# Kernel optimization log

Measured on AMD Instinct MI355X. Metric: run time of the kernel, lower is better.

The kernel has to match this reference:

```python
import jax, jax.numpy as jnp
import numpy as np

# --- constants matching init_kwargs / input_specs ---
B, T, N, C = 16, 60, 196, 512
SEGS, TOP_K, TOP_M = 10, 6, 12
HEADS = 4
HD = C // HEADS  # 128
CLIP = T // SEGS  # 6
FRAMES = CLIP * TOP_K  # 36
LN_EPS = 1e-5


def setup_inputs() -> dict:
    key = jax.random.key(0)
    ks = jax.random.split(key, 16)
    s = 0.02
    return {
        "audio_feat": jax.random.normal(ks[0], (B, T, C), jnp.float32),
        "patch_feat": jax.random.normal(ks[1], (B, T, N, C), jnp.float32),
        "qst_feat": jax.random.normal(ks[2], (B, C), jnp.float32),
        "top_k_index_sort": jnp.sort(jax.random.randint(ks[3], (B, 1, TOP_K), 0, SEGS), axis=-1),
        # MultiheadAttention params (torch layout: in_proj [3C, C])
        "in_proj_w": jax.random.normal(ks[4], (3 * C, C), jnp.float32) * s,
        "in_proj_b": jnp.zeros((3 * C,), jnp.float32),
        "out_w": jax.random.normal(ks[5], (C, C), jnp.float32) * s,
        "out_b": jnp.zeros((C,), jnp.float32),
        # FFN
        "lin1_w": jax.random.normal(ks[6], (C, C), jnp.float32) * s,
        "lin1_b": jnp.zeros((C,), jnp.float32),
        "lin2_w": jax.random.normal(ks[7], (C, C), jnp.float32) * s,
        "lin2_b": jnp.zeros((C,), jnp.float32),
        # LayerNorm
        "ln_g": jnp.ones((C,), jnp.float32),
        "ln_b": jnp.zeros((C,), jnp.float32),
    }


def _layernorm(x, g, b):
    mu = jnp.mean(x, axis=-1, keepdims=True)
    var = jnp.mean(jnp.square(x - mu), axis=-1, keepdims=True)
    return (x - mu) * jax.lax.rsqrt(var + LN_EPS) * g + b


def _forward(audio_feat, patch_feat, qst_feat, top_k_index_sort,
             in_proj_w, in_proj_b, out_w, out_b,
             lin1_w, lin1_b, lin2_w, lin2_b, ln_g, ln_b):
    # --- TopKSegs: gather top-k temporal segments (clip_len frames each) ---
    seg_idx = top_k_index_sort[:, 0, :]  # [B, K]
    frame_ids = (seg_idx[:, :, None] * CLIP + jnp.arange(CLIP)[None, None, :]).reshape(B, FRAMES)
    audio_top_k = jnp.take_along_axis(audio_feat, frame_ids[:, :, None], axis=1)            # [B, F, C]
    patch_top_k = jnp.take_along_axis(patch_feat, frame_ids[:, :, None, None], axis=1)      # [B, F, N, C]

    # --- QstQueryPatchAttn: batched cross-attention (q_len=1 per frame) ---
    Wq, Wk, Wv = in_proj_w[:C], in_proj_w[C:2 * C], in_proj_w[2 * C:]
    bq, bk, bv = in_proj_b[:C], in_proj_b[C:2 * C], in_proj_b[2 * C:]
    q = (qst_feat @ Wq.T + bq).reshape(B, HEADS, HD)                    # [B, h, d]
    k = (patch_top_k @ Wk.T + bk).reshape(B, FRAMES, N, HEADS, HD)      # [B, F, N, h, d]
    v = (patch_top_k @ Wv.T + bv).reshape(B, FRAMES, N, HEADS, HD)
    scale = 1.0 / jnp.sqrt(jnp.asarray(HD, jnp.float32))
    scores = jnp.einsum('bhd,bfnhd->bfhn', q, k) * scale                # [B, F, h, N]
    w = jax.nn.softmax(scores, axis=-1)
    ctx = jnp.einsum('bfhn,bfnhd->bfhd', w, v).reshape(B, FRAMES, C)
    attn_feat = ctx @ out_w.T + out_b                                   # [B, F, C]
    patch_weights = jnp.mean(w, axis=2)                                 # [B, F, N] (avg heads)

    src = jax.nn.relu(attn_feat @ lin1_w.T + lin1_b) @ lin2_w.T + lin2_b
    visual_spatial_feat = _layernorm(attn_feat + src, ln_g, ln_b)       # computed but unused downstream

    # --- SelectTopM (faithful to original loop semantics):
    # top-m indices are sorted ascending and iterated with full-slab overwrite,
    sort_index = jnp.argsort(patch_weights, axis=-1)
    top_m_index = sort_index[:, :, -TOP_M:]
    top_m_index_sort = jnp.sort(top_m_index, axis=-1)
    pid = top_m_index_sort[0, 0, -1]  # last iterated patch id
    sel = jnp.take(patch_top_k, pid, axis=2)                            # [B, F, C]
    visual_patch_top_m = jnp.broadcast_to(sel[:, :, None, :], (B, FRAMES, TOP_M, C))
    visual_patch_feat = visual_patch_top_m.reshape(B, FRAMES * TOP_M, C)
    return audio_top_k, visual_patch_top_m, visual_patch_feat


def reference(audio_feat, patch_feat, qst_feat, top_k_index_sort,
              in_proj_w, in_proj_b, out_w, out_b,
              lin1_w, lin1_b, lin2_w, lin2_b, ln_g, ln_b):
    return _forward(audio_feat, patch_feat, qst_feat, top_k_index_sort,
                    in_proj_w, in_proj_b, out_w, out_b,
                    lin1_w, lin1_b, lin2_w, lin2_b, ln_g, ln_b)
```

## Files before the change

kernel.cpp:

```cpp
#include <hip/hip_runtime.h>
#include <math.h>

#define B_     16
#define T_     60
#define N_     196
#define C_     512
#define SEGS_  10
#define TOPK_  6
#define TOPM_  12
#define HEADS_ 4
#define HD_    128
#define CLIP_  6
#define FRAMES_ 36

#define WS_Q   0
#define WS_SC  512
#define WS_PID 1296

#define SCALE_ 0.08838834764831845f

__global__ void qproj_kernel(const float* __restrict__ qst,
                             const float* __restrict__ ipw,
                             const float* __restrict__ ipb,
                             float* __restrict__ ws) {
    __shared__ float x[C_];
    int tid = threadIdx.x;
    x[tid]       = qst[tid];
    x[tid + 256] = qst[tid + 256];
    __syncthreads();
    const float4* x4 = (const float4*)x;
    for (int r = tid; r < C_; r += 256) {
        const float4* w4 = (const float4*)(ipw + (size_t)r * C_);
        float acc = 0.f;
        #pragma unroll 8
        for (int c = 0; c < C_ / 4; ++c) {
            float4 wv = w4[c], xv = x4[c];
            acc += wv.x * xv.x + wv.y * xv.y + wv.z * xv.z + wv.w * xv.w;
        }
        ws[WS_Q + r] = acc + ipb[r];
    }
}

#define NPER 4
__global__ void score_kernel(const float* __restrict__ patch,
                             const int* __restrict__ tk,
                             const float* __restrict__ ipw,
                             const float* __restrict__ ipb,
                             float* __restrict__ ws) {
    __shared__ float xs[NPER][C_];
    __shared__ float qs[C_];
    __shared__ float kb[NPER][C_];
    int tid = threadIdx.x;
    int n0 = blockIdx.x * NPER;
    int fid0 = tk[0] * CLIP_;
    const size_t base = (size_t)fid0 * N_ * C_;

    qs[tid]       = ws[WS_Q + tid];
    qs[tid + 256] = ws[WS_Q + tid + 256];
    for (int i = tid; i < NPER * C_; i += 256) {
        int n = i >> 9, c = i & (C_ - 1);
        xs[n][c] = patch[base + (size_t)(n0 + n) * C_ + c];
    }
    __syncthreads();

    float a0 = 0.f, a1 = 0.f, a2 = 0.f, a3 = 0.f;
    float b0 = 0.f, b1 = 0.f, b2 = 0.f, b3 = 0.f;
    {
        const float4* w0 = (const float4*)(ipw + (size_t)(C_ + tid) * C_);
        const float4* w1 = (const float4*)(ipw + (size_t)(C_ + tid + 256) * C_);
        const float4* x0 = (const float4*)xs[0];
        const float4* x1 = (const float4*)xs[1];
        const float4* x2 = (const float4*)xs[2];
        const float4* x3 = (const float4*)xs[3];
        for (int c = 0; c < C_ / 4; ++c) {
            float4 wa = w0[c], wb = w1[c];
            float4 v0 = x0[c], v1 = x1[c], v2 = x2[c], v3 = x3[c];
            a0 += wa.x * v0.x + wa.y * v0.y + wa.z * v0.z + wa.w * v0.w;
            a1 += wa.x * v1.x + wa.y * v1.y + wa.z * v1.z + wa.w * v1.w;
            a2 += wa.x * v2.x + wa.y * v2.y + wa.z * v2.z + wa.w * v2.w;
            a3 += wa.x * v3.x + wa.y * v3.y + wa.z * v3.z + wa.w * v3.w;
            b0 += wb.x * v0.x + wb.y * v0.y + wb.z * v0.z + wb.w * v0.w;
            b1 += wb.x * v1.x + wb.y * v1.y + wb.z * v1.z + wb.w * v1.w;
            b2 += wb.x * v2.x + wb.y * v2.y + wb.z * v2.z + wb.w * v2.w;
            b3 += wb.x * v3.x + wb.y * v3.y + wb.z * v3.z + wb.w * v3.w;
        }
    }
    float bk0 = ipb[C_ + tid];
    float bk1 = ipb[C_ + tid + 256];
    kb[0][tid] = a0 + bk0; kb[1][tid] = a1 + bk0;
    kb[2][tid] = a2 + bk0; kb[3][tid] = a3 + bk0;
    kb[0][tid + 256] = b0 + bk1; kb[1][tid + 256] = b1 + bk1;
    kb[2][tid + 256] = b2 + bk1; kb[3][tid + 256] = b3 + bk1;
    __syncthreads();

    int h = tid >> 6, j = tid & 63;
    for (int nn = 0; nn < NPER; ++nn) {
        float p = qs[h * HD_ + j]      * kb[nn][h * HD_ + j]
                + qs[h * HD_ + 64 + j] * kb[nn][h * HD_ + 64 + j];
        for (int off = 32; off; off >>= 1) p += __shfl_down(p, off);
        if (j == 0) ws[WS_SC + h * N_ + n0 + nn] = p * SCALE_;
    }
}

__global__ void pid_kernel(float* __restrict__ ws) {
    __shared__ float wgt[HEADS_][N_];
    __shared__ float pw[N_];
    int tid = threadIdx.x;
    int h = tid >> 6, j = tid & 63;

    float sc[4]; float ex[4];
    int m = 0;
    float mx = -1e30f;
    for (int n = j; n < N_; n += 64) {
        sc[m] = ws[WS_SC + h * N_ + n];
        mx = fmaxf(mx, sc[m]);
        ++m;
    }
    for (int off = 1; off < 64; off <<= 1) mx = fmaxf(mx, __shfl_xor(mx, off));
    float sum = 0.f;
    for (int s = 0; s < m; ++s) { ex[s] = expf(sc[s] - mx); sum += ex[s]; }
    for (int off = 1; off < 64; off <<= 1) sum += __shfl_xor(sum, off);
    float inv = 1.f / sum;
    m = 0;
    for (int n = j; n < N_; n += 64) { wgt[h][n] = ex[m] * inv; ++m; }
    __syncthreads();

    for (int n = tid; n < N_; n += 256)
        pw[n] = 0.25f * (wgt[0][n] + wgt[1][n] + wgt[2][n] + wgt[3][n]);
    __syncthreads();

    if (tid < 64) {
        float v[4];
        for (int s = 0; s < 4; ++s) {
            int n = j + 64 * s;
            v[s] = (n < N_) ? pw[n] : -1e30f;
        }
        int pid = -1;
        for (int r = 0; r < TOPM_; ++r) {
            float bv = -1e30f; int bi = -1;
            for (int s = 0; s < 4; ++s) {
                int n = j + 64 * s;
                if (v[s] > bv || (v[s] == bv && n > bi)) { bv = v[s]; bi = n; }
            }
            for (int off = 1; off < 64; off <<= 1) {
                float ov = __shfl_xor(bv, off);
                int   oi = __shfl_xor(bi, off);
                if (ov > bv || (ov == bv && oi > bi)) { bv = ov; bi = oi; }
            }
            if ((bi & 63) == j) v[bi >> 6] = -1e30f;
            if (bi > pid) pid = bi;
        }
        if (j == 0) ((int*)ws)[WS_PID] = pid;
    }
}

__global__ void out_kernel(const float* __restrict__ audio,
                           const float* __restrict__ patch,
                           const int* __restrict__ tk,
                           const float* __restrict__ ws,
                           float* __restrict__ out) {
    int bf = blockIdx.x;
    int b = bf / FRAMES_, f = bf % FRAMES_;
    int k = f / CLIP_, c = f % CLIP_;
    int fid = tk[b * TOPK_ + k] * CLIP_ + c;
    int t = threadIdx.x;
    int pid = ((const int*)ws)[WS_PID];

    const float4* a4 = (const float4*)(audio + ((size_t)b * T_ + fid) * C_);
    const float4* p4 = (const float4*)(patch + (((size_t)b * T_ + fid) * N_ + pid) * C_);
    float4 av = a4[t];
    float4 sv = p4[t];

    float4* o0 = (float4*)out;
    float4* o1 = (float4*)(out + (size_t)B_ * FRAMES_ * C_);
    float4* o2 = (float4*)(out + (size_t)B_ * FRAMES_ * C_ + (size_t)B_ * FRAMES_ * TOPM_ * C_);

    o0[(size_t)bf * (C_ / 4) + t] = av;
    size_t rb = (size_t)bf * TOPM_ * (C_ / 4);
    #pragma unroll
    for (int mm = 0; mm < TOPM_; ++mm) {
        o1[rb + mm * (C_ / 4) + t] = sv;
        o2[rb + mm * (C_ / 4) + t] = sv;
    }
}

extern "C" void kernel_launch(void* const* d_in, const int* in_sizes, int n_in,
                              void* d_out, int out_size, void* d_ws, size_t ws_size,
                              hipStream_t stream) {
    const float* audio = (const float*)d_in[0];
    const float* patch = (const float*)d_in[1];
    const float* qst   = (const float*)d_in[2];
    const int*   tk    = (const int*)d_in[3];
    const float* ipw   = (const float*)d_in[4];
    const float* ipb   = (const float*)d_in[5];
    float* out = (float*)d_out;
    float* ws  = (float*)d_ws;

    qproj_kernel<<<1, 256, 0, stream>>>(qst, ipw, ipb, ws);
    score_kernel<<<N_ / NPER, 256, 0, stream>>>(patch, tk, ipw, ipb, ws);
    pid_kernel<<<1, 256, 0, stream>>>(ws);
    out_kernel<<<B_ * FRAMES_, 128, 0, stream>>>(audio, patch, tk, ws, out);
}
```

Measured before the change: 529.5 us.

## Fold key projection into query: score patches via q^T Wk instead of full K

```diff
diff --git a/kernel.cpp b/kernel.cpp
--- a/kernel.cpp
+++ b/kernel.cpp
@@ -13,9 +13,9 @@
 #define CLIP_  6
 #define FRAMES_ 36
 
-#define WS_Q   0
-#define WS_SC  512
-#define WS_PID 1296
+#define WS_Q    0
+#define WS_SCP  512
+#define WS_PID  2080
 
 #define SCALE_ 0.08838834764831845f
 
@@ -28,77 +28,56 @@
     x[tid]       = qst[tid];
     x[tid + 256] = qst[tid + 256];
     __syncthreads();
+
+    int wave = tid >> 6, lane = tid & 63;
+    int half = lane >> 5, l = lane & 31;
+    int row = blockIdx.x * 8 + wave * 2 + half;
+
+    const float4* w4 = (const float4*)(ipw + (size_t)row * C_);
     const float4* x4 = (const float4*)x;
-    for (int r = tid; r < C_; r += 256) {
-        const float4* w4 = (const float4*)(ipw + (size_t)r * C_);
-        float acc = 0.f;
-        #pragma unroll 8
-        for (int c = 0; c < C_ / 4; ++c) {
-            float4 wv = w4[c], xv = x4[c];
-            acc += wv.x * xv.x + wv.y * xv.y + wv.z * xv.z + wv.w * xv.w;
-        }
-        ws[WS_Q + r] = acc + ipb[r];
+    float acc = 0.f;
+    #pragma unroll
+    for (int j = 0; j < 4; ++j) {
+        float4 wv = w4[l + 32 * j];
+        float4 xv = x4[l + 32 * j];
+        acc += wv.x * xv.x + wv.y * xv.y + wv.z * xv.z + wv.w * xv.w;
     }
+    for (int off = 16; off; off >>= 1) acc += __shfl_xor(acc, off);
+    if (l == 0) ws[WS_Q + row] = acc + ipb[row];
 }
 
-#define NPER 4
 __global__ void score_kernel(const float* __restrict__ patch,
                              const int* __restrict__ tk,
                              const float* __restrict__ ipw,
-                             const float* __restrict__ ipb,
                              float* __restrict__ ws) {
-    __shared__ float xs[NPER][C_];
-    __shared__ float qs[C_];
-    __shared__ float kb[NPER][C_];
+    __shared__ float qh[HD_];
+    __shared__ float us[256];
     int tid = threadIdx.x;
-    int n0 = blockIdx.x * NPER;
-    int fid0 = tk[0] * CLIP_;
-    const size_t base = (size_t)fid0 * N_ * C_;
+    int h = blockIdx.x >> 1, half = blockIdx.x & 1;
+    int c = half * 256 + tid;
 
-    qs[tid]       = ws[WS_Q + tid];
-    qs[tid + 256] = ws[WS_Q + tid + 256];
-    for (int i = tid; i < NPER * C_; i += 256) {
-        int n = i >> 9, c = i & (C_ - 1);
-        xs[n][c] = patch[base + (size_t)(n0 + n) * C_ + c];
-    }
+    if (tid < HD_) qh[tid] = ws[WS_Q + h * HD_ + tid];
     __syncthreads();
 
-    float a0 = 0.f, a1 = 0.f, a2 = 0.f, a3 = 0.f;
-    float b0 = 0.f, b1 = 0.f, b2 = 0.f, b3 = 0.f;
-    {
-        const float4* w0 = (const float4*)(ipw + (size_t)(C_ + tid) * C_);
-        const float4* w1 = (const float4*)(ipw + (size_t)(C_ + tid + 256) * C_);
-        const float4* x0 = (const float4*)xs[0];
-        const float4* x1 = (const float4*)xs[1];
-        const float4* x2 = (const float4*)xs[2];
-        const float4* x3 = (const float4*)xs[3];
-        for (int c = 0; c < C_ / 4; ++c) {
-            float4 wa = w0[c], wb = w1[c];
-            float4 v0 = x0[c], v1 = x1[c], v2 = x2[c], v3 = x3[c];
-            a0 += wa.x * v0.x + wa.y * v0.y + wa.z * v0.z + wa.w * v0.w;
-            a1 += wa.x * v1.x + wa.y * v1.y + wa.z * v1.z + wa.w * v1.w;
-            a2 += wa.x * v2.x + wa.y * v2.y + wa.z * v2.z + wa.w * v2.w;
-            a3 += wa.x * v3.x + wa.y * v3.y + wa.z * v3.z + wa.w * v3.w;
-            b0 += wb.x * v0.x + wb.y * v0.y + wb.z * v0.z + wb.w * v0.w;
-            b1 += wb.x * v1.x + wb.y * v1.y + wb.z * v1.z + wb.w * v1.w;
-            b2 += wb.x * v2.x + wb.y * v2.y + wb.z * v2.z + wb.w * v2.w;
-            b3 += wb.x * v3.x + wb.y * v3.y + wb.z * v3.z + wb.w * v3.w;
-        }
-    }
-    float bk0 = ipb[C_ + tid];
-    float bk1 = ipb[C_ + tid + 256];
-    kb[0][tid] = a0 + bk0; kb[1][tid] = a1 + bk0;
-    kb[2][tid] = a2 + bk0; kb[3][tid] = a3 + bk0;
-    kb[0][tid + 256] = b0 + bk1; kb[1][tid + 256] = b1 + bk1;
-    kb[2][tid + 256] = b2 + bk1; kb[3][tid + 256] = b3 + bk1;
+    const float* wk = ipw + (size_t)(C_ + h * HD_) * C_ + c;
+    float u = 0.f;
+    #pragma unroll 16
+    for (int d = 0; d < HD_; ++d) u += qh[d] * wk[(size_t)d * C_];
+    us[tid] = u;
     __syncthreads();
 
-    int h = tid >> 6, j = tid & 63;
-    for (int nn = 0; nn < NPER; ++nn) {
-        float p = qs[h * HD_ + j]      * kb[nn][h * HD_ + j]
-                + qs[h * HD_ + 64 + j] * kb[nn][h * HD_ + 64 + j];
+    int fid0 = tk[0] * CLIP_;
+    const float* pb = patch + (size_t)fid0 * N_ * C_ + half * 256;
+    int wave = tid >> 6, lane = tid & 63;
+    const float4* u4 = (const float4*)us;
+    float4 uv = u4[lane];
+    for (int n = wave; n < N_; n += 4) {
+        const float4* x4 = (const float4*)(pb + (size_t)n * C_);
+        float4 xv = x4[lane];
+        float p = uv.x * xv.x + uv.y * xv.y + uv.z * xv.z + uv.w * xv.w;
         for (int off = 32; off; off >>= 1) p += __shfl_down(p, off);
-        if (j == 0) ws[WS_SC + h * N_ + n0 + nn] = p * SCALE_;
+        if (lane == 0)
+            ws[WS_SCP + (size_t)blockIdx.x * N_ + n] = p * SCALE_;
     }
 }
 
@@ -112,7 +91,8 @@
     int m = 0;
     float mx = -1e30f;
     for (int n = j; n < N_; n += 64) {
-        sc[m] = ws[WS_SC + h * N_ + n];
+        sc[m] = ws[WS_SCP + (size_t)(2 * h) * N_ + n]
+              + ws[WS_SCP + (size_t)(2 * h + 1) * N_ + n];
         mx = fmaxf(mx, sc[m]);
         ++m;
     }
@@ -196,8 +176,8 @@
     float* out = (float*)d_out;
     float* ws  = (float*)d_ws;
 
-    qproj_kernel<<<1, 256, 0, stream>>>(qst, ipw, ipb, ws);
-    score_kernel<<<N_ / NPER, 256, 0, stream>>>(patch, tk, ipw, ipb, ws);
+    qproj_kernel<<<64, 256, 0, stream>>>(qst, ipw, ipb, ws);
+    score_kernel<<<8, 256, 0, stream>>>(patch, tk, ipw, ws);
     pid_kernel<<<1, 256, 0, stream>>>(ws);
     out_kernel<<<B_ * FRAMES_, 128, 0, stream>>>(audio, patch, tk, ws, out);
 }
```

New measurement: 497.1 us. 6.1% less time.
